# Optimization experiments

Hardware: AMD Instinct MI355X
Metric: run time of the kernel (lower is better)

Reference implementation:

```python
import jax, jax.numpy as jnp
import numpy as np

DIM = 512
NUM_HEADS = 8
HEAD_DIM = DIM // NUM_HEADS
SCALE = HEAD_DIM ** -0.5
B, N = 8, 1024


def setup_inputs() -> dict:
    key = jax.random.key(0)
    k1, k2, k3, k4, k5 = jax.random.split(key, 5)
    x = jax.random.normal(k1, (B, N, DIM), dtype=jnp.float32)
    rpe_bias = jax.random.normal(k2, (1, NUM_HEADS, N, N), dtype=jnp.float32)
    # torch Linear weights: [out_features, in_features], y = x @ W.T
    qkv_w = jax.random.normal(k3, (3 * DIM, DIM), dtype=jnp.float32) * (DIM ** -0.5)
    proj_w = jax.random.normal(k4, (DIM, DIM), dtype=jnp.float32) * (DIM ** -0.5)
    proj_b = jax.random.normal(k5, (DIM,), dtype=jnp.float32) * 0.01
    return {"x": x, "rpe_bias": rpe_bias, "qkv_w": qkv_w, "proj_w": proj_w, "proj_b": proj_b}


def reference(x, rpe_bias, qkv_w, proj_w, proj_b):
    b, n, c = x.shape
    h, d = NUM_HEADS, HEAD_DIM
    # qkv projection (no bias): [B,N,3C] -> [3,B,H,N,D]
    qkv = (x @ qkv_w.T).reshape(b, n, 3, h, d).transpose(2, 0, 3, 1, 4)
    q, k, v = qkv[0], qkv[1], qkv[2]
    attn = jnp.einsum('bhnd,bhmd->bhnm', q, k) * SCALE + rpe_bias
    attn = jax.nn.softmax(attn, axis=-1)  # dropout p=0 -> identity
    out = jnp.einsum('bhnm,bhmd->bhnd', attn, v)
    out = out.transpose(0, 2, 1, 3).reshape(b, n, c)
    return out @ proj_w.T + proj_b
```

## Files before the change

kernel.cpp:

```cpp
#include <hip/hip_runtime.h>
#include <hip/hip_bf16.h>

#define B_    8
#define N_    1024
#define DIM_  512
#define H_    8
#define DH_   64
#define SCALE_ 0.125f

typedef unsigned short u16;
typedef __attribute__((ext_vector_type(8))) short bf16x8;
typedef __attribute__((ext_vector_type(4))) short bf16x4;
typedef __attribute__((ext_vector_type(4))) float f32x4;

__device__ __forceinline__ u16 f2bf(float f) {
  union { float f; unsigned u; } v; v.f = f;
  return (u16)((v.u + 0x7fffu + ((v.u >> 16) & 1u)) >> 16);
}
__device__ __forceinline__ unsigned pack2(float a, float b) {
  return (unsigned)f2bf(a) | ((unsigned)f2bf(b) << 16);
}
__device__ __forceinline__ void cp16(const void* g, void* l) {
  __builtin_amdgcn_global_load_lds(
      (const __attribute__((address_space(1))) unsigned*)g,
      (__attribute__((address_space(3))) unsigned*)l, 16, 0, 0);
}

__global__ __launch_bounds__(256) void convert_kernel(
    const float* __restrict__ X, const float* __restrict__ Wq,
    const float* __restrict__ Wp, u16* __restrict__ Xb,
    u16* __restrict__ Wqb, u16* __restrict__ Wpb) {
  const int NX4 = (B_ * N_ * DIM_) / 4;
  const int NQ4 = (3 * DIM_ * DIM_) / 4;
  const int NP4 = (DIM_ * DIM_) / 4;
  const int total = NX4 + NQ4 + NP4;
  const int stride = gridDim.x * 256;
  for (int i = blockIdx.x * 256 + threadIdx.x; i < total; i += stride) {
    const float* s; u16* d; int off;
    if (i < NX4)            { s = X;  d = Xb;  off = i; }
    else if (i < NX4 + NQ4) { s = Wq; d = Wqb; off = i - NX4; }
    else                    { s = Wp; d = Wpb; off = i - NX4 - NQ4; }
    float4 f = *(const float4*)(s + (size_t)off * 4);
    uint2 u; u.x = pack2(f.x, f.y); u.y = pack2(f.z, f.w);
    *(uint2*)(d + (size_t)off * 4) = u;
  }
}

__global__ __launch_bounds__(256, 4) void qkv_gemm(
    const u16* __restrict__ Ab, const u16* __restrict__ Bb,
    u16* __restrict__ Q, u16* __restrict__ K, u16* __restrict__ Vt) {
  __shared__ __align__(16) u16 sA[128 * 64];
  __shared__ __align__(16) u16 sB[64 * 64];
  const int t = threadIdx.x;
  const int wv = t >> 6, lane = t & 63, quad = (lane >> 4) & 3, l15 = lane & 15;
  const int m0 = blockIdx.y * 128;
  const int n0 = blockIdx.x * 64;

  const int srow = lane >> 3;
  const int schunk = (lane & 7) ^ srow;
  const size_t ga = (size_t)(m0 + srow) * DIM_ + schunk * 8;
  const size_t gb = (size_t)(n0 + srow) * DIM_ + schunk * 8;

  f32x4 zero = {0.f, 0.f, 0.f, 0.f};
  f32x4 acc[2][4];
#pragma unroll
  for (int i = 0; i < 2; i++)
#pragma unroll
    for (int j = 0; j < 4; j++) acc[i][j] = zero;

  for (int k0 = 0; k0 < DIM_; k0 += 64) {
    __syncthreads();
#pragma unroll
    for (int i = 0; i < 4; i++) {
      const int rb = 32 * wv + 8 * i;
      cp16(Ab + ga + (size_t)rb * DIM_ + k0, &sA[rb * 64]);
    }
#pragma unroll
    for (int i = 0; i < 2; i++) {
      const int rb = 16 * wv + 8 * i;
      cp16(Bb + gb + (size_t)rb * DIM_ + k0, &sB[rb * 64]);
    }
    __syncthreads();
#pragma unroll
    for (int ks = 0; ks < 2; ks++) {
      bf16x8 af[2], bfv[4];
#pragma unroll
      for (int i = 0; i < 2; i++)
        af[i] = *(const bf16x8*)&sA[(wv * 32 + 16 * i + l15) * 64 +
                                    (((ks << 2) | quad) ^ (l15 & 7)) * 8];
#pragma unroll
      for (int j = 0; j < 4; j++)
        bfv[j] = *(const bf16x8*)&sB[(16 * j + l15) * 64 +
                                     (((ks << 2) | quad) ^ (l15 & 7)) * 8];
#pragma unroll
      for (int i = 0; i < 2; i++)
#pragma unroll
        for (int j = 0; j < 4; j++)
          acc[i][j] = __builtin_amdgcn_mfma_f32_16x16x32_bf16(af[i], bfv[j], acc[i][j], 0, 0, 0);
    }
  }

  const int tsel = n0 >> 9;
#pragma unroll
  for (int j = 0; j < 4; j++) {
    const int jg = n0 + 16 * j + l15;
    const int h = (jg >> 6) & 7, d = jg & 63;
#pragma unroll
    for (int i = 0; i < 2; i++) {
      const int mbase = m0 + wv * 32 + 16 * i + quad * 4;
      const int b = mbase >> 10, nb = mbase & 1023;
      const size_t bh = (size_t)(b * H_ + h);
      if (tsel == 2) {
        ushort4 v4;
        v4.x = f2bf(acc[i][j][0]); v4.y = f2bf(acc[i][j][1]);
        v4.z = f2bf(acc[i][j][2]); v4.w = f2bf(acc[i][j][3]);
        *(ushort4*)&Vt[(bh * DH_ + d) * N_ + nb] = v4;
      } else {
        u16* dst = (tsel == 0 ? Q : K);
#pragma unroll
        for (int rr = 0; rr < 4; rr++)
          dst[(bh * N_ + nb + rr) * DH_ + d] = f2bf(acc[i][j][rr]);
      }
    }
  }
}

__global__ __launch_bounds__(256, 4) void attn_kernel(
    const u16* __restrict__ Q, const u16* __restrict__ K,
    const u16* __restrict__ Vt, const float* __restrict__ bias,
    u16* __restrict__ AO) {
  __shared__ __align__(16) u16 sK[64 * 64];
  __shared__ __align__(16) u16 sV[64 * 64];
  const int t = threadIdx.x;
  const int wv = t >> 6, lane = t & 63, quad = (lane >> 4) & 3, l15 = lane & 15;

  const int bid = blockIdx.x;
  const int h = bid & 7;
  const int s = bid >> 3;
  const int nx = s >> 3;
  const int b = s & 7;
  const int n0 = nx << 6;
  const int bh = b * H_ + h;
  const int r = t >> 2, c = (t & 3) << 4;

  const int qg = n0 + 16 * wv + l15;
  bf16x8 qf0, qf1;
  {
    const u16* qa = Q + (((size_t)bh << 10) + qg) * DH_ + (quad << 3);
    qf0 = *(const bf16x8*)qa; qf1 = *(const bf16x8*)(qa + 32);
  }

  const float* bp = bias + (((size_t)h << 10) + qg) * N_ + (quad << 2);
  const u16* kbase = K + (((size_t)bh << 10) + r) * DH_ + c;
  const u16* vbase = Vt + (((size_t)bh << 6) + r) * N_ + c;

  const int so0 = r * 128 + ((((t & 3) << 5)) ^ ((r & 7) << 4));
  const int so1 = r * 128 + ((((t & 3) << 5) + 16) ^ ((r & 7) << 4));
  const int rx = (l15 & 7) << 4;
  const int frow = l15 * 128;
  const int vhalf = (quad & 1) << 3;

  f32x4 zero = {0.f, 0.f, 0.f, 0.f};
  f32x4 O[4];
  O[0] = zero; O[1] = zero; O[2] = zero; O[3] = zero;
  float lsum = 0.f;

  uint4 k0r = *(const uint4*)kbase, k1r = *(const uint4*)(kbase + 8);
  uint4 v0r = *(const uint4*)vbase, v1r = *(const uint4*)(vbase + 8);

  for (int kt = 0; kt < 16; kt++) {
    __syncthreads();
    *(uint4*)((char*)sK + so0) = k0r; *(uint4*)((char*)sK + so1) = k1r;
    *(uint4*)((char*)sV + so0) = v0r; *(uint4*)((char*)sV + so1) = v1r;
    if (kt < 15) {
      const u16* kn = kbase + (size_t)(kt + 1) * 64 * DH_;
      const u16* vn = vbase + (kt + 1) * 64;
      k0r = *(const uint4*)kn; k1r = *(const uint4*)(kn + 8);
      v0r = *(const uint4*)vn; v1r = *(const uint4*)(vn + 8);
    }
    float4 b4[4];
#pragma unroll
    for (int cb = 0; cb < 4; cb++)
      b4[cb] = *(const float4*)(bp + (kt << 6) + 16 * cb);
    __syncthreads();

    bf16x8 kf[8];
#pragma unroll
    for (int ks = 0; ks < 2; ks++)
#pragma unroll
      for (int cb = 0; cb < 4; cb++)
        kf[ks * 4 + cb] = *(const bf16x8*)((const char*)sK + cb * 2048 + frow +
                                           (((ks << 6) | (quad << 4)) ^ rx));

    f32x4 S[4];
    S[0] = zero; S[1] = zero; S[2] = zero; S[3] = zero;
    __builtin_amdgcn_s_setprio(1);
#pragma unroll
    for (int ks = 0; ks < 2; ks++) {
      const bf16x8 qf = ks ? qf1 : qf0;
#pragma unroll
      for (int cb = 0; cb < 4; cb++)
        S[cb] = __builtin_amdgcn_mfma_f32_16x16x32_bf16(kf[ks * 4 + cb], qf, S[cb], 0, 0, 0);
    }
    __builtin_amdgcn_s_setprio(0);

    bf16x4 p[4];
#pragma unroll
    for (int cb = 0; cb < 4; cb++) {
      float p0 = __expf(fmaf(S[cb][0], SCALE_, b4[cb].x));
      float p1 = __expf(fmaf(S[cb][1], SCALE_, b4[cb].y));
      float p2 = __expf(fmaf(S[cb][2], SCALE_, b4[cb].z));
      float p3 = __expf(fmaf(S[cb][3], SCALE_, b4[cb].w));
      lsum += (p0 + p1) + (p2 + p3);
      uint2 pk; pk.x = pack2(p0, p1); pk.y = pack2(p2, p3);
      p[cb] = __builtin_bit_cast(bf16x4, pk);
    }

    __builtin_amdgcn_s_setprio(1);
#pragma unroll
    for (int cbp = 0; cbp < 4; cbp++) {
      bf16x4 vf[4];
#pragma unroll
      for (int cb = 0; cb < 4; cb++) {
        const int ch = ((((2 * cb + (quad >> 1)) << 4)) ^ rx) + vhalf;
        vf[cb] = *(const bf16x4*)((const char*)sV + cbp * 2048 + frow + ch);
      }
#pragma unroll
      for (int cb = 0; cb < 4; cb++)
        O[cbp] = __builtin_amdgcn_mfma_f32_16x16x16bf16_1k(vf[cb], p[cb], O[cbp], 0, 0, 0);
    }
    __builtin_amdgcn_s_setprio(0);
  }

  lsum += __shfl_xor(lsum, 16);
  lsum += __shfl_xor(lsum, 32);
  const float inv = 1.f / lsum;
#pragma unroll
  for (int cb = 0; cb < 4; cb++) {
    ushort4 o4;
    o4.x = f2bf(O[cb][0] * inv); o4.y = f2bf(O[cb][1] * inv);
    o4.z = f2bf(O[cb][2] * inv); o4.w = f2bf(O[cb][3] * inv);
    *(ushort4*)&AO[(((size_t)bh << 10 | (size_t)0) * 0) +
                   (((size_t)b << 10) + qg) * DIM_ + h * DH_ + 16 * cb + (quad << 2)] = o4;
  }
}

__global__ __launch_bounds__(256, 4) void proj_gemm(
    const u16* __restrict__ Ab, const u16* __restrict__ Bb,
    const float* __restrict__ Pb, float* __restrict__ Out) {
  __shared__ __align__(16) u16 sA[128 * 64];
  __shared__ __align__(16) u16 sB[64 * 64];
  const int t = threadIdx.x;
  const int wv = t >> 6, lane = t & 63, quad = (lane >> 4) & 3, l15 = lane & 15;
  const int m0 = blockIdx.y * 128;
  const int n0 = blockIdx.x * 64;

  const int srow = lane >> 3;
  const int schunk = (lane & 7) ^ srow;
  const size_t ga = (size_t)(m0 + srow) * DIM_ + schunk * 8;
  const size_t gb = (size_t)(n0 + srow) * DIM_ + schunk * 8;

  f32x4 zero = {0.f, 0.f, 0.f, 0.f};
  f32x4 acc[2][4];
#pragma unroll
  for (int i = 0; i < 2; i++)
#pragma unroll
    for (int j = 0; j < 4; j++) acc[i][j] = zero;

  for (int k0 = 0; k0 < DIM_; k0 += 64) {
    __syncthreads();
#pragma unroll
    for (int i = 0; i < 4; i++) {
      const int rb = 32 * wv + 8 * i;
      cp16(Ab + ga + (size_t)rb * DIM_ + k0, &sA[rb * 64]);
    }
#pragma unroll
    for (int i = 0; i < 2; i++) {
      const int rb = 16 * wv + 8 * i;
      cp16(Bb + gb + (size_t)rb * DIM_ + k0, &sB[rb * 64]);
    }
    __syncthreads();
#pragma unroll
    for (int ks = 0; ks < 2; ks++) {
      bf16x8 af[2], bfv[4];
#pragma unroll
      for (int i = 0; i < 2; i++)
        af[i] = *(const bf16x8*)&sA[(wv * 32 + 16 * i + l15) * 64 +
                                    (((ks << 2) | quad) ^ (l15 & 7)) * 8];
#pragma unroll
      for (int j = 0; j < 4; j++)
        bfv[j] = *(const bf16x8*)&sB[(16 * j + l15) * 64 +
                                     (((ks << 2) | quad) ^ (l15 & 7)) * 8];
#pragma unroll
      for (int i = 0; i < 2; i++)
#pragma unroll
        for (int j = 0; j < 4; j++)
          acc[i][j] = __builtin_amdgcn_mfma_f32_16x16x32_bf16(af[i], bfv[j], acc[i][j], 0, 0, 0);
    }
  }

#pragma unroll
  for (int j = 0; j < 4; j++) {
    const int jg = n0 + 16 * j + l15;
    const float pb = Pb[jg];
#pragma unroll
    for (int i = 0; i < 2; i++) {
      const int mbase = m0 + wv * 32 + 16 * i + quad * 4;
#pragma unroll
      for (int rr = 0; rr < 4; rr++)
        Out[(size_t)(mbase + rr) * DIM_ + jg] = acc[i][j][rr] + pb;
    }
  }
}

extern "C" void kernel_launch(void* const* d_in, const int* in_sizes, int n_in,
                              void* d_out, int out_size, void* d_ws, size_t ws_size,
                              hipStream_t stream) {
  const float* x      = (const float*)d_in[0];
  const float* rpe    = (const float*)d_in[1];
  const float* qkv_w  = (const float*)d_in[2];
  const float* proj_w = (const float*)d_in[3];
  const float* proj_b = (const float*)d_in[4];
  float* out = (float*)d_out;

  const size_t perbuf = (size_t)B_ * N_ * DIM_;
  u16* Xb  = (u16*)d_ws;
  u16* Q   = Xb + perbuf;
  u16* K   = Q + perbuf;
  u16* Vt  = K + perbuf;
  u16* Wqb = Vt + perbuf;
  u16* Wpb = Wqb + (size_t)3 * DIM_ * DIM_;
  u16* AO  = Xb;

  convert_kernel<<<2560, 256, 0, stream>>>(x, qkv_w, proj_w, Xb, Wqb, Wpb);
  qkv_gemm<<<dim3(24, 64), 256, 0, stream>>>(Xb, Wqb, Q, K, Vt);
  attn_kernel<<<1024, 256, 0, stream>>>(Q, K, Vt, rpe, AO);
  proj_gemm<<<dim3(8, 64), 256, 0, stream>>>(AO, Wpb, proj_b, out);
}
```

Baseline: 173.7 us.

## Fuse X conversion into QKV GEMM, widen attention blocks, vectorize epilogue stores

The standalone fp32-to-bf16 conversion of X is dropped. The QKV GEMM now loads fp32 X into registers, converts it, and writes it to LDS with a one-tile register prefetch. Q/K and the proj output epilogues swap MFMA operands so each lane writes contiguous 4-element vectors instead of scalar strided stores. The attention kernel moves to 512-thread blocks covering 128 queries that share each K/V tile, halving K/V reloads per query. The trade-off is more register pressure in the GEMM and fewer, larger attention blocks.

```diff
diff --git a/kernel.cpp b/kernel.cpp
--- a/kernel.cpp
+++ b/kernel.cpp
@@ -13,6 +13,9 @@
 typedef __attribute__((ext_vector_type(4))) short bf16x4;
 typedef __attribute__((ext_vector_type(4))) float f32x4;
 
+struct SwTrue  { static constexpr bool value = true;  };
+struct SwFalse { static constexpr bool value = false; };
+
 __device__ __forceinline__ u16 f2bf(float f) {
   union { float f; unsigned u; } v; v.f = f;
   return (u16)((v.u + 0x7fffu + ((v.u >> 16) & 1u)) >> 16);
@@ -27,27 +30,23 @@
 }
 
 __global__ __launch_bounds__(256) void convert_kernel(
-    const float* __restrict__ X, const float* __restrict__ Wq,
-    const float* __restrict__ Wp, u16* __restrict__ Xb,
+    const float* __restrict__ Wq, const float* __restrict__ Wp,
     u16* __restrict__ Wqb, u16* __restrict__ Wpb) {
-  const int NX4 = (B_ * N_ * DIM_) / 4;
   const int NQ4 = (3 * DIM_ * DIM_) / 4;
   const int NP4 = (DIM_ * DIM_) / 4;
-  const int total = NX4 + NQ4 + NP4;
-  const int stride = gridDim.x * 256;
-  for (int i = blockIdx.x * 256 + threadIdx.x; i < total; i += stride) {
-    const float* s; u16* d; int off;
-    if (i < NX4)            { s = X;  d = Xb;  off = i; }
-    else if (i < NX4 + NQ4) { s = Wq; d = Wqb; off = i - NX4; }
-    else                    { s = Wp; d = Wpb; off = i - NX4 - NQ4; }
-    float4 f = *(const float4*)(s + (size_t)off * 4);
-    uint2 u; u.x = pack2(f.x, f.y); u.y = pack2(f.z, f.w);
-    *(uint2*)(d + (size_t)off * 4) = u;
-  }
+  const int total = NQ4 + NP4;
+  const int i = blockIdx.x * 256 + threadIdx.x;
+  if (i >= total) return;
+  const float* s; u16* d; int off;
+  if (i < NQ4) { s = Wq; d = Wqb; off = i; }
+  else         { s = Wp; d = Wpb; off = i - NQ4; }
+  float4 f = *(const float4*)(s + (size_t)off * 4);
+  uint2 u; u.x = pack2(f.x, f.y); u.y = pack2(f.z, f.w);
+  *(uint2*)(d + (size_t)off * 4) = u;
 }
 
 __global__ __launch_bounds__(256, 4) void qkv_gemm(
-    const u16* __restrict__ Ab, const u16* __restrict__ Bb,
+    const float* __restrict__ X, const u16* __restrict__ Bb,
     u16* __restrict__ Q, u16* __restrict__ K, u16* __restrict__ Vt) {
   __shared__ __align__(16) u16 sA[128 * 64];
   __shared__ __align__(16) u16 sB[64 * 64];
@@ -56,10 +55,15 @@
   const int m0 = blockIdx.y * 128;
   const int n0 = blockIdx.x * 64;
 
+  const int xr = t >> 3, xc = t & 7;
+  const float* xsrc = X + (size_t)(m0 + xr) * DIM_ + ((xc ^ (xr & 7)) << 3);
+  u16* xdst = &sA[xr * 64 + xc * 8];
+
   const int srow = lane >> 3;
   const int schunk = (lane & 7) ^ srow;
-  const size_t ga = (size_t)(m0 + srow) * DIM_ + schunk * 8;
   const size_t gb = (size_t)(n0 + srow) * DIM_ + schunk * 8;
+
+  const int tsel = n0 >> 9;
 
   f32x4 zero = {0.f, 0.f, 0.f, 0.f};
   f32x4 acc[2][4];
@@ -68,80 +72,119 @@
 #pragma unroll
     for (int j = 0; j < 4; j++) acc[i][j] = zero;
 
-  for (int k0 = 0; k0 < DIM_; k0 += 64) {
-    __syncthreads();
-#pragma unroll
-    for (int i = 0; i < 4; i++) {
-      const int rb = 32 * wv + 8 * i;
-      cp16(Ab + ga + (size_t)rb * DIM_ + k0, &sA[rb * 64]);
-    }
-#pragma unroll
-    for (int i = 0; i < 2; i++) {
-      const int rb = 16 * wv + 8 * i;
-      cp16(Bb + gb + (size_t)rb * DIM_ + k0, &sB[rb * 64]);
-    }
-    __syncthreads();
-#pragma unroll
-    for (int ks = 0; ks < 2; ks++) {
-      bf16x8 af[2], bfv[4];
-#pragma unroll
-      for (int i = 0; i < 2; i++)
-        af[i] = *(const bf16x8*)&sA[(wv * 32 + 16 * i + l15) * 64 +
-                                    (((ks << 2) | quad) ^ (l15 & 7)) * 8];
-#pragma unroll
-      for (int j = 0; j < 4; j++)
-        bfv[j] = *(const bf16x8*)&sB[(16 * j + l15) * 64 +
-                                     (((ks << 2) | quad) ^ (l15 & 7)) * 8];
-#pragma unroll
-      for (int i = 0; i < 2; i++)
+  float4 xf[4][2];
+#pragma unroll
+  for (int ii = 0; ii < 4; ii++) {
+    const float* p = xsrc + (size_t)ii * 32 * DIM_;
+    xf[ii][0] = *(const float4*)p;
+    xf[ii][1] = *(const float4*)(p + 4);
+  }
+
+  auto kloop = [&](auto swv) {
+    constexpr bool SW = decltype(swv)::value;
+    for (int k0 = 0; k0 < DIM_; k0 += 64) {
+      __syncthreads();
+#pragma unroll
+      for (int ii = 0; ii < 4; ii++) {
+        uint4 u;
+        u.x = pack2(xf[ii][0].x, xf[ii][0].y);
+        u.y = pack2(xf[ii][0].z, xf[ii][0].w);
+        u.z = pack2(xf[ii][1].x, xf[ii][1].y);
+        u.w = pack2(xf[ii][1].z, xf[ii][1].w);
+        *(uint4*)(xdst + ii * 32 * 64) = u;
+      }
+#pragma unroll
+      for (int i = 0; i < 2; i++) {
+        const int rb = 16 * wv + 8 * i;
+        cp16(Bb + gb + (size_t)rb * DIM_ + k0, &sB[rb * 64]);
+      }
+      if (k0 < DIM_ - 64) {
+#pragma unroll
+        for (int ii = 0; ii < 4; ii++) {
+          const float* p = xsrc + (size_t)ii * 32 * DIM_ + k0 + 64;
+          xf[ii][0] = *(const float4*)p;
+          xf[ii][1] = *(const float4*)(p + 4);
+        }
+      }
+      __syncthreads();
+#pragma unroll
+      for (int ks = 0; ks < 2; ks++) {
+        bf16x8 af[2], bfv[4];
+#pragma unroll
+        for (int i = 0; i < 2; i++)
+          af[i] = *(const bf16x8*)&sA[(wv * 32 + 16 * i + l15) * 64 +
+                                      (((ks << 2) | quad) ^ (l15 & 7)) * 8];
 #pragma unroll
         for (int j = 0; j < 4; j++)
-          acc[i][j] = __builtin_amdgcn_mfma_f32_16x16x32_bf16(af[i], bfv[j], acc[i][j], 0, 0, 0);
-    }
-  }
-
-  const int tsel = n0 >> 9;
-#pragma unroll
-  for (int j = 0; j < 4; j++) {
-    const int jg = n0 + 16 * j + l15;
-    const int h = (jg >> 6) & 7, d = jg & 63;
-#pragma unroll
-    for (int i = 0; i < 2; i++) {
-      const int mbase = m0 + wv * 32 + 16 * i + quad * 4;
-      const int b = mbase >> 10, nb = mbase & 1023;
-      const size_t bh = (size_t)(b * H_ + h);
-      if (tsel == 2) {
+          bfv[j] = *(const bf16x8*)&sB[(16 * j + l15) * 64 +
+                                       (((ks << 2) | quad) ^ (l15 & 7)) * 8];
+#pragma unroll
+        for (int i = 0; i < 2; i++)
+#pragma unroll
+          for (int j = 0; j < 4; j++) {
+            if (SW)
+              acc[i][j] = __builtin_amdgcn_mfma_f32_16x16x32_bf16(bfv[j], af[i], acc[i][j], 0, 0, 0);
+            else
+              acc[i][j] = __builtin_amdgcn_mfma_f32_16x16x32_bf16(af[i], bfv[j], acc[i][j], 0, 0, 0);
+          }
+      }
+    }
+  };
+
+  const int h = (n0 >> 6) & 7;
+  if (tsel == 2) {
+    kloop(SwFalse{});
+#pragma unroll
+    for (int j = 0; j < 4; j++) {
+      const int d = 16 * j + l15;
+#pragma unroll
+      for (int i = 0; i < 2; i++) {
+        const int mbase = m0 + wv * 32 + 16 * i + (quad << 2);
+        const int b = mbase >> 10, nb = mbase & 1023;
+        const size_t bh = (size_t)(b * H_ + h);
         ushort4 v4;
         v4.x = f2bf(acc[i][j][0]); v4.y = f2bf(acc[i][j][1]);
         v4.z = f2bf(acc[i][j][2]); v4.w = f2bf(acc[i][j][3]);
         *(ushort4*)&Vt[(bh * DH_ + d) * N_ + nb] = v4;
-      } else {
-        u16* dst = (tsel == 0 ? Q : K);
-#pragma unroll
-        for (int rr = 0; rr < 4; rr++)
-          dst[(bh * N_ + nb + rr) * DH_ + d] = f2bf(acc[i][j][rr]);
-      }
-    }
-  }
-}
-
-__global__ __launch_bounds__(256, 4) void attn_kernel(
+      }
+    }
+  } else {
+    kloop(SwTrue{});
+    u16* dst = (tsel == 0) ? Q : K;
+#pragma unroll
+    for (int j = 0; j < 4; j++) {
+      const int d = 16 * j + (quad << 2);
+#pragma unroll
+      for (int i = 0; i < 2; i++) {
+        const int m = m0 + wv * 32 + 16 * i + l15;
+        const int b = m >> 10, nb = m & 1023;
+        const size_t bh = (size_t)(b * H_ + h);
+        ushort4 v4;
+        v4.x = f2bf(acc[i][j][0]); v4.y = f2bf(acc[i][j][1]);
+        v4.z = f2bf(acc[i][j][2]); v4.w = f2bf(acc[i][j][3]);
+        *(ushort4*)&dst[(bh * N_ + nb) * DH_ + d] = v4;
+      }
+    }
+  }
+}
+
+__global__ __launch_bounds__(512, 4) void attn_kernel(
     const u16* __restrict__ Q, const u16* __restrict__ K,
     const u16* __restrict__ Vt, const float* __restrict__ bias,
     u16* __restrict__ AO) {
   __shared__ __align__(16) u16 sK[64 * 64];
   __shared__ __align__(16) u16 sV[64 * 64];
   const int t = threadIdx.x;
-  const int wv = t >> 6, lane = t & 63, quad = (lane >> 4) & 3, l15 = lane & 15;
+  const int wv = t >> 6;
+  const int lane = t & 63, quad = (lane >> 4) & 3, l15 = lane & 15;
 
   const int bid = blockIdx.x;
   const int h = bid & 7;
   const int s = bid >> 3;
   const int nx = s >> 3;
   const int b = s & 7;
-  const int n0 = nx << 6;
+  const int n0 = nx << 7;
   const int bh = b * H_ + h;
-  const int r = t >> 2, c = (t & 3) << 4;
 
   const int qg = n0 + 16 * wv + l15;
   bf16x8 qf0, qf1;
@@ -151,11 +194,12 @@
   }
 
   const float* bp = bias + (((size_t)h << 10) + qg) * N_ + (quad << 2);
-  const u16* kbase = K + (((size_t)bh << 10) + r) * DH_ + c;
-  const u16* vbase = Vt + (((size_t)bh << 6) + r) * N_ + c;
-
-  const int so0 = r * 128 + ((((t & 3) << 5)) ^ ((r & 7) << 4));
-  const int so1 = r * 128 + ((((t & 3) << 5) + 16) ^ ((r & 7) << 4));
+
+  const int r = t >> 3, c8 = t & 7;
+  const u16* kbase = K + (((size_t)bh << 10) + r) * DH_ + (c8 << 3);
+  const u16* vbase = Vt + (((size_t)bh << 6) + r) * N_ + (c8 << 3);
+  const int so = r * 128 + ((c8 ^ (r & 7)) << 4);
+
   const int rx = (l15 & 7) << 4;
   const int frow = l15 * 128;
   const int vhalf = (quad & 1) << 3;
@@ -165,18 +209,16 @@
   O[0] = zero; O[1] = zero; O[2] = zero; O[3] = zero;
   float lsum = 0.f;
 
-  uint4 k0r = *(const uint4*)kbase, k1r = *(const uint4*)(kbase + 8);
-  uint4 v0r = *(const uint4*)vbase, v1r = *(const uint4*)(vbase + 8);
+  uint4 kr = *(const uint4*)kbase;
+  uint4 vr = *(const uint4*)vbase;
 
   for (int kt = 0; kt < 16; kt++) {
     __syncthreads();
-    *(uint4*)((char*)sK + so0) = k0r; *(uint4*)((char*)sK + so1) = k1r;
-    *(uint4*)((char*)sV + so0) = v0r; *(uint4*)((char*)sV + so1) = v1r;
+    *(uint4*)((char*)sK + so) = kr;
+    *(uint4*)((char*)sV + so) = vr;
     if (kt < 15) {
-      const u16* kn = kbase + (size_t)(kt + 1) * 64 * DH_;
-      const u16* vn = vbase + (kt + 1) * 64;
-      k0r = *(const uint4*)kn; k1r = *(const uint4*)(kn + 8);
-      v0r = *(const uint4*)vn; v1r = *(const uint4*)(vn + 8);
+      kr = *(const uint4*)(kbase + (size_t)(kt + 1) * 64 * DH_);
+      vr = *(const uint4*)(vbase + (kt + 1) * 64);
     }
     float4 b4[4];
 #pragma unroll
@@ -240,8 +282,7 @@
     ushort4 o4;
     o4.x = f2bf(O[cb][0] * inv); o4.y = f2bf(O[cb][1] * inv);
     o4.z = f2bf(O[cb][2] * inv); o4.w = f2bf(O[cb][3] * inv);
-    *(ushort4*)&AO[(((size_t)bh << 10 | (size_t)0) * 0) +
-                   (((size_t)b << 10) + qg) * DIM_ + h * DH_ + 16 * cb + (quad << 2)] = o4;
+    *(ushort4*)&AO[(((size_t)b << 10) + qg) * DIM_ + h * DH_ + 16 * cb + (quad << 2)] = o4;
   }
 }
 
@@ -295,20 +336,21 @@
       for (int i = 0; i < 2; i++)
 #pragma unroll
         for (int j = 0; j < 4; j++)
-          acc[i][j] = __builtin_amdgcn_mfma_f32_16x16x32_bf16(af[i], bfv[j], acc[i][j], 0, 0, 0);
+          acc[i][j] = __builtin_amdgcn_mfma_f32_16x16x32_bf16(bfv[j], af[i], acc[i][j], 0, 0, 0);
     }
   }
 
 #pragma unroll
   for (int j = 0; j < 4; j++) {
-    const int jg = n0 + 16 * j + l15;
-    const float pb = Pb[jg];
+    const int col = n0 + 16 * j + (quad << 2);
+    const float4 pb4 = *(const float4*)&Pb[col];
 #pragma unroll
     for (int i = 0; i < 2; i++) {
-      const int mbase = m0 + wv * 32 + 16 * i + quad * 4;
-#pragma unroll
-      for (int rr = 0; rr < 4; rr++)
-        Out[(size_t)(mbase + rr) * DIM_ + jg] = acc[i][j][rr] + pb;
+      const int m = m0 + wv * 32 + 16 * i + l15;
+      float4 o;
+      o.x = acc[i][j][0] + pb4.x; o.y = acc[i][j][1] + pb4.y;
+      o.z = acc[i][j][2] + pb4.z; o.w = acc[i][j][3] + pb4.w;
+      *(float4*)&Out[(size_t)m * DIM_ + col] = o;
     }
   }
 }
@@ -324,16 +366,15 @@
   float* out = (float*)d_out;
 
   const size_t perbuf = (size_t)B_ * N_ * DIM_;
-  u16* Xb  = (u16*)d_ws;
-  u16* Q   = Xb + perbuf;
+  u16* AO  = (u16*)d_ws;
+  u16* Q   = AO + perbuf;
   u16* K   = Q + perbuf;
   u16* Vt  = K + perbuf;
   u16* Wqb = Vt + perbuf;
   u16* Wpb = Wqb + (size_t)3 * DIM_ * DIM_;
-  u16* AO  = Xb;
-
-  convert_kernel<<<2560, 256, 0, stream>>>(x, qkv_w, proj_w, Xb, Wqb, Wpb);
-  qkv_gemm<<<dim3(24, 64), 256, 0, stream>>>(Xb, Wqb, Q, K, Vt);
-  attn_kernel<<<1024, 256, 0, stream>>>(Q, K, Vt, rpe, AO);
+
+  convert_kernel<<<1024, 256, 0, stream>>>(qkv_w, proj_w, Wqb, Wpb);
+  qkv_gemm<<<dim3(24, 64), 256, 0, stream>>>(x, Wqb, Q, K, Vt);
+  attn_kernel<<<512, 512, 0, stream>>>(Q, K, Vt, rpe, AO);
   proj_gemm<<<dim3(8, 64), 256, 0, stream>>>(AO, Wpb, proj_b, out);
 }
```

Result: slower. 192.2 us (+10.7%).
